# Optimization experiments

Measured on AMD Instinct MI355X. Metric: run time of the kernel, lower is better.

The kernel has to match this reference:

```python
import jax, jax.numpy as jnp
import numpy as np

PARAM = 10  # half of last dim of x

def _metrik(two_p):
    m = np.zeros((two_p, two_p), dtype=np.float32)
    m[4, 4] = 1.0
    m[5, 5] = 1.0
    return jnp.asarray(m)

def setup_inputs() -> dict:
    key = jax.random.key(0)
    B, gs, two_p = 8, 512, 2 * PARAM
    x = jax.random.normal(key, (B, gs, two_p), dtype=jnp.float32)
    return {"x": x, "free": 30}

def reference(x, free):
    B, gs, two_p = x.shape
    p = two_p // 2
    M = _metrik(two_p)
    # pairwise difference: diff[b,i,j,k] = x[b,i,k] - x[b,j,k]
    diff = x[:, :, None, :] - x[:, None, :, :]          # (B, gs, gs, 2p)
    # squared Mahalanobis distance (quadratic form with constant metric M)
    dsq = jnp.einsum('bijk,kl,bijl->bij', diff, M, diff)  # (B, gs, gs)
    basegraph = jnp.exp(-dsq)
    parax = x[:, :, p:]                                  # (B, gs, p)
    if free == 0:
        return jnp.concatenate((basegraph, parax), axis=-1)
    zeros = jnp.zeros((B, gs, free), dtype=x.dtype)
    return jnp.concatenate((basegraph, parax, zeros), axis=-1)
```

## Files before the change

kernel.cpp:

```cpp
#include <hip/hip_runtime.h>


#define GS    512
#define TWO_P 20
#define P     10
#define FREE  30
#define ROWW  (GS + P + FREE)

__global__ __launch_bounds__(GS) void gbuilder_kernel(const float* __restrict__ x,
                                                      float* __restrict__ out) {
    const int row = blockIdx.x;
    const int b   = row >> 9;
    const int i   = row & (GS - 1);
    const int j   = threadIdx.x;

    const float* xb = x + (size_t)b * GS * TWO_P;

    const float2 xi = *reinterpret_cast<const float2*>(xb + (size_t)i * TWO_P + 4);
    const float2 xj = *reinterpret_cast<const float2*>(xb + (size_t)j * TWO_P + 4);

    const float d4 = xi.x - xj.x;
    const float d5 = xi.y - xj.y;
    const float dsq = d4 * d4 + d5 * d5;

    float* orow = out + (size_t)row * ROWW;
    orow[j] = __expf(-dsq);

    if (j < P + FREE) {
        orow[GS + j] = (j < P) ? xb[(size_t)i * TWO_P + P + j] : 0.0f;
    }
}

extern "C" void kernel_launch(void* const* d_in, const int* in_sizes, int n_in,
                              void* d_out, int out_size, void* d_ws, size_t ws_size,
                              hipStream_t stream) {
    const float* x = (const float*)d_in[0];
    float* out = (float*)d_out;
    gbuilder_kernel<<<8 * GS, GS, 0, stream>>>(x, out);
}
```

Before: 12.04 us.

## Process eight rows per block with float4 vectorized stores

Each block of 256 threads now covers 8 output rows instead of one row per 512-thread block. Each thread computes 16 outputs and writes them as four float4 stores, and the tail (parax plus zeros) is also written with float4 stores. The aim is fewer launched blocks and wider global stores for this write-bound kernel. Row width 542 floats is not a multiple of 4, so float4 stores to odd rows are misaligned, which is a correctness or performance risk.

```diff
diff --git a/kernel.cpp b/kernel.cpp
--- a/kernel.cpp
+++ b/kernel.cpp
@@ -4,30 +4,51 @@
 #define GS    512
 #define TWO_P 20
 #define P     10
-#define FREE  30
-#define ROWW  (GS + P + FREE)
+#define ROWW  (GS + P + 30)
+#define TPB   256
+#define RPB   8
 
-__global__ __launch_bounds__(GS) void gbuilder_kernel(const float* __restrict__ x,
-                                                      float* __restrict__ out) {
-    const int row = blockIdx.x;
-    const int b   = row >> 9;
-    const int i   = row & (GS - 1);
-    const int j   = threadIdx.x;
+__global__ __launch_bounds__(TPB) void gbuilder_kernel(const float* __restrict__ x,
+                                                       float* __restrict__ out) {
+    const int row0 = blockIdx.x * RPB;
+    const int b    = row0 >> 9;
+    const int t    = threadIdx.x;
 
     const float* xb = x + (size_t)b * GS * TWO_P;
 
-    const float2 xi = *reinterpret_cast<const float2*>(xb + (size_t)i * TWO_P + 4);
-    const float2 xj = *reinterpret_cast<const float2*>(xb + (size_t)j * TWO_P + 4);
+    const int r  = t >> 5;
+    const int i  = (row0 & (GS - 1)) + r;
+    const float2 xi = *reinterpret_cast<const float2*>(xb + i * TWO_P + 4);
 
-    const float d4 = xi.x - xj.x;
-    const float d5 = xi.y - xj.y;
-    const float dsq = d4 * d4 + d5 * d5;
+    float* orow = out + (size_t)(row0 + r) * ROWW;
+    const int jb = (t & 31) * 4;
 
-    float* orow = out + (size_t)row * ROWW;
-    orow[j] = __expf(-dsq);
+    #pragma unroll
+    for (int q = 0; q < 4; ++q) {
+        float4 v;
+        #pragma unroll
+        for (int k = 0; k < 4; ++k) {
+            const int j = jb + 128 * q + k;
+            const float2 xj = *reinterpret_cast<const float2*>(xb + j * TWO_P + 4);
+            const float d4 = xi.x - xj.x;
+            const float d5 = xi.y - xj.y;
+            (&v.x)[k] = __expf(-(d4 * d4 + d5 * d5));
+        }
+        *reinterpret_cast<float4*>(orow + jb + 128 * q) = v;
+    }
 
-    if (j < P + FREE) {
-        orow[GS + j] = (j < P) ? xb[(size_t)i * TWO_P + P + j] : 0.0f;
+    if (t < 80) {
+        const int rr = t / 10;
+        const int s  = t % 10;
+        const int ii = (row0 & (GS - 1)) + rr;
+        const float* xrow = xb + ii * TWO_P;
+        float4 tail = make_float4(0.f, 0.f, 0.f, 0.f);
+        #pragma unroll
+        for (int q = 0; q < 4; ++q) {
+            const int m = 4 * s + q;
+            if (m < P) (&tail.x)[q] = xrow[P + m];
+        }
+        *reinterpret_cast<float4*>(out + (size_t)(row0 + rr) * ROWW + GS + 4 * s) = tail;
     }
 }
 
@@ -36,5 +57,5 @@
                               hipStream_t stream) {
     const float* x = (const float*)d_in[0];
     float* out = (float*)d_out;
-    gbuilder_kernel<<<8 * GS, GS, 0, stream>>>(x, out);
+    gbuilder_kernel<<<(8 * GS) / RPB, TPB, 0, stream>>>(x, out);
 }
```

Result: faster. 10.46 us (-13.2%).
